# Kernel tuning notes

Hardware: AMD Instinct MI355X
Metric: run time of the kernel (lower is better)

Reference implementation:

```python
import jax, jax.numpy as jnp
import numpy as np

N_NODES = 100000
N_EDGES = 1250000
D_IN = 64
D_HID = 64
N_CLS = 40


def setup_inputs() -> dict:
    key = jax.random.key(0)
    ks = jax.random.split(key, 8)
    x = jax.random.normal(ks[0], (N_NODES, D_IN), dtype=jnp.float32)
    edge_index = jax.random.randint(ks[1], (2, N_EDGES), 0, N_NODES, dtype=jnp.int64)
    s = 1.0 / np.sqrt(D_IN)
    W1_l = jax.random.normal(ks[2], (D_IN, D_HID), dtype=jnp.float32) * s
    W1_r = jax.random.normal(ks[3], (D_IN, D_HID), dtype=jnp.float32) * s
    b1 = jnp.zeros((D_HID,), dtype=jnp.float32)
    s2 = 1.0 / np.sqrt(D_HID)
    W2_l = jax.random.normal(ks[4], (D_HID, N_CLS), dtype=jnp.float32) * s2
    W2_r = jax.random.normal(ks[5], (D_HID, N_CLS), dtype=jnp.float32) * s2
    b2 = jnp.zeros((N_CLS,), dtype=jnp.float32)
    return {"x": x, "edge_index": edge_index, "W1_l": W1_l, "b1": b1,
            "W1_r": W1_r, "W2_l": W2_l, "b2": b2, "W2_r": W2_r}


def _sage_conv(h, src, dst, n_nodes, W_l, b, W_r):
    # mean-aggregate neighbor features: out[i] = mean_{(j->i)} h[j]
    msg = h[src]                                             # [E, d] gather
    agg = jax.ops.segment_sum(msg, dst, num_segments=n_nodes)  # [N, d] scatter-add
    deg = jax.ops.segment_sum(jnp.ones_like(dst, dtype=h.dtype), dst,
                              num_segments=n_nodes)
    agg = agg / jnp.maximum(deg, 1.0)[:, None]
    # lin_l(aggregated, bias) + lin_r(root, no bias)
    return agg @ W_l + b + h @ W_r


def reference(x, edge_index, W1_l, b1, W1_r, W2_l, b2, W2_r):
    n = x.shape[0]
    src, dst = edge_index[0], edge_index[1]
    h = jax.nn.relu(_sage_conv(x, src, dst, n, W1_l, b1, W1_r))
    # dropout is identity in eval mode (training=False)
    h = _sage_conv(h, src, dst, n, W2_l, b2, W2_r)
    return jax.nn.log_softmax(h, axis=1)
```

## Files before the change

kernel.cpp:

```cpp
#include <hip/hip_runtime.h>
#include <hip/hip_bf16.h>
#include <math.h>

#define N_NODES 100000
#define N_EDGES 1250000
#define D_IN    64
#define D_HID   64
#define N_CLS   40

#define NBUCK      500
#define BUCK_NODES 200
#define BUCK_CAP   2944
#define NBLK_STAGE 512
#define NBLK_GEMM1 1024
#define ELL_W      44
#define GNODES     100

typedef unsigned int uint;
typedef __attribute__((ext_vector_type(8))) short bf16x8;
typedef __attribute__((ext_vector_type(4))) float f32x4;

static __device__ __forceinline__ uint pack_bf16x2(float a, float b) {
    unsigned short ua = __builtin_bit_cast(unsigned short, __float2bfloat16(a));
    unsigned short ub = __builtin_bit_cast(unsigned short, __float2bfloat16(b));
    return (uint)ua | ((uint)ub << 16);
}
static __device__ __forceinline__ short f2bf(float f) {
    return (short)__builtin_bit_cast(unsigned short, __float2bfloat16(f));
}

__global__ __launch_bounds__(256, 3) void stage_and_gemm1(
    const int* __restrict__ src, const int* __restrict__ dst,
    int* __restrict__ bucketCnt, uint* __restrict__ staged,
    const float* __restrict__ x,
    const float* __restrict__ W_l, const float* __restrict__ W_r,
    const float* __restrict__ b,
    __hip_bfloat16* __restrict__ y1, __hip_bfloat16* __restrict__ r1,
    int ntiles)
{
    __shared__ int cntB[NBUCK], offB[NBUCK], gbase[NBUCK];

    if (blockIdx.x < NBLK_STAGE) {
        const int per = (N_EDGES + NBLK_STAGE - 1) / NBLK_STAGE;
        const int e0 = blockIdx.x * per;
        const int e1 = (e0 + per < N_EDGES) ? e0 + per : N_EDGES;
        for (int i = threadIdx.x; i < NBUCK; i += 256) { cntB[i] = 0; offB[i] = 0; }
        __syncthreads();
        for (int e = e0 + threadIdx.x; e < e1; e += 256)
            atomicAdd(&cntB[dst[e] / BUCK_NODES], 1);
        __syncthreads();
        for (int i = threadIdx.x; i < NBUCK; i += 256) {
            int c = cntB[i];
            gbase[i] = c ? atomicAdd(&bucketCnt[i], c) : 0;
        }
        __syncthreads();
        for (int e = e0 + threadIdx.x; e < e1; e += 256) {
            int d = dst[e];
            int s = src[e];
            int bk = d / BUCK_NODES;
            int pos = gbase[bk] + atomicAdd(&offB[bk], 1);
            if (pos < BUCK_CAP)
                staged[(size_t)bk * BUCK_CAP + pos] =
                    (uint)s | ((uint)(d - bk * BUCK_NODES) << 17);
        }
        return;
    }

    const int gbid = blockIdx.x - NBLK_STAGE;
    if (gbid == 0 && threadIdx.x < 64)
        y1[(size_t)N_NODES * 64 + threadIdx.x] = __float2bfloat16(0.0f);

    const int lane = threadIdx.x & 63;
    const int m = lane & 15;
    const int q = lane >> 4;

    bf16x8 bfrag[8][2];
    float  biasv[4];
    #pragma unroll
    for (int t = 0; t < 8; ++t) {
        const float* Wsrc = (t < 4) ? W_l : W_r;
        const int c = t * 16 + m - ((t < 4) ? 0 : 64);
        #pragma unroll
        for (int ks = 0; ks < 2; ++ks) {
            bf16x8 f;
            #pragma unroll
            for (int j = 0; j < 8; ++j)
                f[j] = f2bf(Wsrc[(ks * 32 + q * 8 + j) * 64 + c]);
            bfrag[t][ks] = f;
        }
    }
    #pragma unroll
    for (int t = 0; t < 4; ++t) biasv[t] = b[t * 16 + m];

    int wid = gbid * 4 + (threadIdx.x >> 6);
    const int nw = NBLK_GEMM1 * 4;
    for (int tile = wid; tile < ntiles; tile += nw) {
        const int node0 = tile * 16;
        const float* xrow = x + (size_t)(node0 + m) * 64 + q * 8;
        bf16x8 afrag[2];
        #pragma unroll
        for (int ks = 0; ks < 2; ++ks) {
            float4 f0 = *(const float4*)(xrow + ks * 32);
            float4 f1 = *(const float4*)(xrow + ks * 32 + 4);
            bf16x8 a;
            a[0] = f2bf(f0.x); a[1] = f2bf(f0.y); a[2] = f2bf(f0.z); a[3] = f2bf(f0.w);
            a[4] = f2bf(f1.x); a[5] = f2bf(f1.y); a[6] = f2bf(f1.z); a[7] = f2bf(f1.w);
            afrag[ks] = a;
        }
        f32x4 acc[8];
        #pragma unroll
        for (int t = 0; t < 8; ++t) acc[t] = (f32x4){0.f, 0.f, 0.f, 0.f};
        #pragma unroll
        for (int ks = 0; ks < 2; ++ks) {
            #pragma unroll
            for (int t = 0; t < 8; ++t)
                acc[t] = __builtin_amdgcn_mfma_f32_16x16x32_bf16(
                    afrag[ks], bfrag[t][ks], acc[t], 0, 0, 0);
        }
        #pragma unroll
        for (int t = 0; t < 8; ++t) {
            #pragma unroll
            for (int r = 0; r < 4; ++r) {
                const size_t row = (size_t)(node0 + q * 4 + r);
                if (t < 4)
                    y1[row * 64 + t * 16 + m] = __float2bfloat16(acc[t][r]);
                else
                    r1[row * 64 + (t - 4) * 16 + m] =
                        __float2bfloat16(acc[t][r] + biasv[t - 4]);
            }
        }
    }
}

__global__ __launch_bounds__(512) void bucket_gather1(
    const __hip_bfloat16* __restrict__ y1,
    const uint* __restrict__ staged, const int* __restrict__ bucketCnt,
    __hip_bfloat16* __restrict__ h)
{
    __shared__ int lcnt[GNODES];
    __shared__ int lslots[GNODES * ELL_W + 64];
    const int pb = blockIdx.x >> 1;
    const int hf = blockIdx.x & 1;
    const int node0 = pb * BUCK_NODES + hf * GNODES;

    for (int i = threadIdx.x; i < GNODES; i += 512) lcnt[i] = 0;
    __syncthreads();

    int total = bucketCnt[pb]; if (total > BUCK_CAP) total = BUCK_CAP;
    const uint* sp = staged + (size_t)pb * BUCK_CAP;
    const int rel0 = hf * GNODES;
    for (int i = threadIdx.x; i < total; i += 512) {
        uint v = sp[i];
        int rel = (int)(v >> 17) - rel0;
        if (0 <= rel && rel < GNODES) {
            int pos = atomicAdd(&lcnt[rel], 1);
            if (pos < ELL_W) lslots[rel * ELL_W + pos] = (int)(v & 0x1FFFFu);
        }
    }
    __syncthreads();

    const int lane = threadIdx.x & 63;
    const int wv   = threadIdx.x >> 6;
    const int q4   = (lane >> 4) * 4;
    const int pre  = (lane & 15) * 8;
    const char* y1c = (const char*)y1;

    for (int n = wv; n < GNODES; n += 8) {
        const int node = node0 + n;
        const int degr = lcnt[n];
        const int idxv = lslots[n * ELL_W + lane];
        const int degc = degr < ELL_W ? degr : ELL_W;
        int idx = (lane >= degc) ? N_NODES : idxv;

        float a0 = 0.f, a1 = 0.f, a2 = 0.f, a3 = 0.f;
        const int groups = (degc + 15) & ~15;
        for (int e = 0; e < groups; e += 16) {
            int sel0 = __builtin_amdgcn_ds_bpermute(e * 4      + q4, idx);
            int sel1 = __builtin_amdgcn_ds_bpermute(e * 4 + 16 + q4, idx);
            int sel2 = __builtin_amdgcn_ds_bpermute(e * 4 + 32 + q4, idx);
            int sel3 = __builtin_amdgcn_ds_bpermute(e * 4 + 48 + q4, idx);
            uint2 d0 = *(const uint2*)(y1c + ((size_t)(uint)sel0 * 128u + (uint)pre));
            uint2 d1 = *(const uint2*)(y1c + ((size_t)(uint)sel1 * 128u + (uint)pre));
            uint2 d2 = *(const uint2*)(y1c + ((size_t)(uint)sel2 * 128u + (uint)pre));
            uint2 d3 = *(const uint2*)(y1c + ((size_t)(uint)sel3 * 128u + (uint)pre));
            a0 += __uint_as_float(d0.x << 16) + __uint_as_float(d1.x << 16)
                + __uint_as_float(d2.x << 16) + __uint_as_float(d3.x << 16);
            a1 += __uint_as_float(d0.x & 0xffff0000u) + __uint_as_float(d1.x & 0xffff0000u)
                + __uint_as_float(d2.x & 0xffff0000u) + __uint_as_float(d3.x & 0xffff0000u);
            a2 += __uint_as_float(d0.y << 16) + __uint_as_float(d1.y << 16)
                + __uint_as_float(d2.y << 16) + __uint_as_float(d3.y << 16);
            a3 += __uint_as_float(d0.y & 0xffff0000u) + __uint_as_float(d1.y & 0xffff0000u)
                + __uint_as_float(d2.y & 0xffff0000u) + __uint_as_float(d3.y & 0xffff0000u);
        }
        a0 += __shfl_xor(a0, 16); a0 += __shfl_xor(a0, 32);
        a1 += __shfl_xor(a1, 16); a1 += __shfl_xor(a1, 32);
        a2 += __shfl_xor(a2, 16); a2 += __shfl_xor(a2, 32);
        a3 += __shfl_xor(a3, 16); a3 += __shfl_xor(a3, 32);

        uint2 rr = *(const uint2*)((const char*)h + ((size_t)node * 128u + (uint)pre));
        float r0  = __uint_as_float(rr.x << 16);
        float r1v = __uint_as_float(rr.x & 0xffff0000u);
        float r2v = __uint_as_float(rr.y << 16);
        float r3  = __uint_as_float(rr.y & 0xffff0000u);

        float inv = 1.0f / (float)(degr > 1 ? degr : 1);
        float v0 = a0 * inv + r0;  v0 = v0 > 0.f ? v0 : 0.f;
        float v1 = a1 * inv + r1v; v1 = v1 > 0.f ? v1 : 0.f;
        float v2 = a2 * inv + r2v; v2 = v2 > 0.f ? v2 : 0.f;
        float v3 = a3 * inv + r3;  v3 = v3 > 0.f ? v3 : 0.f;

        if (lane < 16) {
            uint2 o;
            o.x = pack_bf16x2(v0, v1);
            o.y = pack_bf16x2(v2, v3);
            *(uint2*)((char*)h + ((size_t)node * 128u + (uint)pre)) = o;
        }
    }
}

__global__ __launch_bounds__(256, 3) void gemm2_mfma(
    const __hip_bfloat16* __restrict__ h,
    const float* __restrict__ W_l, const float* __restrict__ W_r,
    const float* __restrict__ b,
    __hip_bfloat16* __restrict__ y2, __hip_bfloat16* __restrict__ r2,
    int ntiles)
{
    if (blockIdx.x == 0 && threadIdx.x < N_CLS)
        y2[(size_t)N_NODES * N_CLS + threadIdx.x] = __float2bfloat16(0.0f);

    const int lane = threadIdx.x & 63;
    const int m = lane & 15;
    const int q = lane >> 4;

    bf16x8 bfrag[5][2];
    float  biasv[5];
    #pragma unroll
    for (int t = 0; t < 5; ++t) {
        const int g = t * 16 + m;
        const float* Wsrc = (g < N_CLS) ? W_l : W_r;
        const int c = (g < N_CLS) ? g : g - N_CLS;
        #pragma unroll
        for (int ks = 0; ks < 2; ++ks) {
            bf16x8 f;
            #pragma unroll
            for (int j = 0; j < 8; ++j)
                f[j] = f2bf(Wsrc[(ks * 32 + q * 8 + j) * N_CLS + c]);
            bfrag[t][ks] = f;
        }
        biasv[t] = (g >= N_CLS) ? b[g - N_CLS] : 0.0f;
    }

    int wid = blockIdx.x * 4 + (threadIdx.x >> 6);
    const int nw = gridDim.x * 4;
    for (int tile = wid; tile < ntiles; tile += nw) {
        const int node0 = tile * 16;
        const __hip_bfloat16* hrow = h + (size_t)(node0 + m) * 64 + q * 8;
        bf16x8 afrag[2];
        afrag[0] = *(const bf16x8*)(hrow);
        afrag[1] = *(const bf16x8*)(hrow + 32);
        f32x4 acc[5];
        #pragma unroll
        for (int t = 0; t < 5; ++t) acc[t] = (f32x4){0.f, 0.f, 0.f, 0.f};
        #pragma unroll
        for (int ks = 0; ks < 2; ++ks) {
            #pragma unroll
            for (int t = 0; t < 5; ++t)
                acc[t] = __builtin_amdgcn_mfma_f32_16x16x32_bf16(
                    afrag[ks], bfrag[t][ks], acc[t], 0, 0, 0);
        }
        #pragma unroll
        for (int t = 0; t < 5; ++t) {
            const int g = t * 16 + m;
            #pragma unroll
            for (int r = 0; r < 4; ++r) {
                const size_t row = (size_t)(node0 + q * 4 + r);
                float v = acc[t][r] + biasv[t];
                if (g < N_CLS) y2[row * N_CLS + g] = __float2bfloat16(v);
                else           r2[row * N_CLS + (g - N_CLS)] = __float2bfloat16(v);
            }
        }
    }
}

__global__ __launch_bounds__(512) void bucket_gather2(
    const __hip_bfloat16* __restrict__ y2,
    const __hip_bfloat16* __restrict__ r2,
    const uint* __restrict__ staged, const int* __restrict__ bucketCnt,
    float* __restrict__ out)
{
    __shared__ int lcnt[GNODES];
    __shared__ int lslots[GNODES * ELL_W + 64];
    const int pb = blockIdx.x >> 1;
    const int hf = blockIdx.x & 1;
    const int node0 = pb * BUCK_NODES + hf * GNODES;

    for (int i = threadIdx.x; i < GNODES; i += 512) lcnt[i] = 0;
    __syncthreads();

    int total = bucketCnt[pb]; if (total > BUCK_CAP) total = BUCK_CAP;
    const uint* sp = staged + (size_t)pb * BUCK_CAP;
    const int rel0 = hf * GNODES;
    for (int i = threadIdx.x; i < total; i += 512) {
        uint v = sp[i];
        int rel = (int)(v >> 17) - rel0;
        if (0 <= rel && rel < GNODES) {
            int pos = atomicAdd(&lcnt[rel], 1);
            if (pos < ELL_W) lslots[rel * ELL_W + pos] = (int)(v & 0x1FFFFu);
        }
    }
    __syncthreads();

    const int lane  = threadIdx.x & 63;
    const int wv    = threadIdx.x >> 6;
    const int lpair = lane & 31;
    const int p2    = (lane >> 5) * 4;
    const uint pre2 = (uint)(lpair < 20 ? lpair : 19) * 4u;
    const char* y2c = (const char*)y2;

    for (int n = wv; n < GNODES; n += 8) {
        const int node = node0 + n;
        const int degr = lcnt[n];
        const int idxv = lslots[n * ELL_W + lane];
        const int degc = degr < ELL_W ? degr : ELL_W;
        int idx = (lane >= degc) ? N_NODES : idxv;

        float a0 = 0.f, a1 = 0.f;
        const int groups = (degc + 7) & ~7;
        for (int e = 0; e < groups; e += 8) {
            int sel0 = __builtin_amdgcn_ds_bpermute(e * 4      + p2, idx);
            int sel1 = __builtin_amdgcn_ds_bpermute(e * 4 +  8 + p2, idx);
            int sel2 = __builtin_amdgcn_ds_bpermute(e * 4 + 16 + p2, idx);
            int sel3 = __builtin_amdgcn_ds_bpermute(e * 4 + 24 + p2, idx);
            uint d0 = *(const uint*)(y2c + ((size_t)(uint)sel0 * 80u + pre2));
            uint d1 = *(const uint*)(y2c + ((size_t)(uint)sel1 * 80u + pre2));
            uint d2 = *(const uint*)(y2c + ((size_t)(uint)sel2 * 80u + pre2));
            uint d3 = *(const uint*)(y2c + ((size_t)(uint)sel3 * 80u + pre2));
            a0 += __uint_as_float(d0 << 16) + __uint_as_float(d1 << 16)
                + __uint_as_float(d2 << 16) + __uint_as_float(d3 << 16);
            a1 += __uint_as_float(d0 & 0xffff0000u) + __uint_as_float(d1 & 0xffff0000u)
                + __uint_as_float(d2 & 0xffff0000u) + __uint_as_float(d3 & 0xffff0000u);
        }
        a0 += __shfl_xor(a0, 32);
        a1 += __shfl_xor(a1, 32);

        uint rr = *(const uint*)((const char*)r2 + ((size_t)node * 80u + pre2));
        float r0 = __uint_as_float(rr << 16);
        float r1 = __uint_as_float(rr & 0xffff0000u);

        float inv = 1.0f / (float)(degr > 1 ? degr : 1);
        float l0 = a0 * inv + r0;
        float l1 = a1 * inv + r1;
        if (lpair >= 20) { l0 = -INFINITY; l1 = -INFINITY; }

        float m = fmaxf(l0, l1);
        #pragma unroll
        for (int off = 16; off > 0; off >>= 1)
            m = fmaxf(m, __shfl_xor(m, off));
        float ex = (lpair < 20) ? (expf(l0 - m) + expf(l1 - m)) : 0.0f;
        #pragma unroll
        for (int off = 16; off > 0; off >>= 1)
            ex += __shfl_xor(ex, off);
        float lg = m + logf(ex);
        if (lane < 20) {
            float2 o = make_float2(l0 - lg, l1 - lg);
            *(float2*)(out + (size_t)node * N_CLS + lpair * 2) = o;
        }
    }
}

extern "C" void kernel_launch(void* const* d_in, const int* in_sizes, int n_in,
                              void* d_out, int out_size, void* d_ws, size_t ws_size,
                              hipStream_t stream)
{
    (void)in_sizes; (void)n_in; (void)out_size; (void)ws_size;

    const float* x    = (const float*)d_in[0];
    const int*   ei   = (const int*)d_in[1];
    const float* W1_l = (const float*)d_in[2];
    const float* b1   = (const float*)d_in[3];
    const float* W1_r = (const float*)d_in[4];
    const float* W2_l = (const float*)d_in[5];
    const float* b2   = (const float*)d_in[6];
    const float* W2_r = (const float*)d_in[7];
    float* out = (float*)d_out;

    const int* src = ei;
    const int* dst = ei + N_EDGES;

    char* ws = (char*)d_ws;
    int*            bucketCnt = (int*)(ws);
    uint*           staged    = (uint*)(ws + (1u << 20));
    __hip_bfloat16* y1        = (__hip_bfloat16*)(ws + 8388608u);
    __hip_bfloat16* y2        = (__hip_bfloat16*)(ws + 8388608u);
    __hip_bfloat16* h         = (__hip_bfloat16*)(ws + 22020096u);
    __hip_bfloat16* r2        = (__hip_bfloat16*)(ws + 35651584u);

    const int ntiles = N_NODES / 16;

    hipMemsetAsync(bucketCnt, 0, NBUCK * sizeof(int), stream);
    stage_and_gemm1<<<NBLK_STAGE + NBLK_GEMM1, 256, 0, stream>>>(
        src, dst, bucketCnt, staged, x, W1_l, W1_r, b1, y1, h, ntiles);

    bucket_gather1<<<NBUCK * 2, 512, 0, stream>>>(y1, staged, bucketCnt, h);

    gemm2_mfma<<<1024, 256, 0, stream>>>(h, W2_l, W2_r, b2, y2, r2, ntiles);

    bucket_gather2<<<NBUCK * 2, 512, 0, stream>>>(y2, r2, staged, bucketCnt, out);
}
```

Baseline: 194.0 us.

## Fuse layer-1 gather with layer-2 GEMM via LDS and add dynamic tile scheduling

Merges the layer-1 neighbor aggregation and the layer-2 MFMA GEMM into one kernel. Each block writes its 128 aggregated hidden rows into padded LDS and multiplies them there, so h no longer makes a round trip through global memory and one launch is dropped. Buckets grow to 256 nodes so bucket indexing becomes a shift. Staging blocks now also join the GEMM1 tile loop, which pulls tiles from an atomic counter. The cost is extra LDS per block, which may lower occupancy, and bounds checks for the partial last bucket.

```diff
diff --git a/kernel.cpp b/kernel.cpp
--- a/kernel.cpp
+++ b/kernel.cpp
@@ -8,13 +8,14 @@
 #define D_HID   64
 #define N_CLS   40
 
-#define NBUCK      500
-#define BUCK_NODES 200
-#define BUCK_CAP   2944
+#define NBUCK      391
+#define BUCK_NODES 256
+#define BUCK_CAP   3712
 #define NBLK_STAGE 512
 #define NBLK_GEMM1 1024
 #define ELL_W      44
-#define GNODES     100
+#define GNODES     128
+#define HPAD       80
 
 typedef unsigned int uint;
 typedef __attribute__((ext_vector_type(8))) short bf16x8;
@@ -31,12 +32,13 @@
 
 __global__ __launch_bounds__(256, 3) void stage_and_gemm1(
     const int* __restrict__ src, const int* __restrict__ dst,
-    int* __restrict__ bucketCnt, uint* __restrict__ staged,
+    int* __restrict__ bucketCnt, int* __restrict__ tileCtr,
+    uint* __restrict__ staged,
     const float* __restrict__ x,
     const float* __restrict__ W_l, const float* __restrict__ W_r,
     const float* __restrict__ b,
     __hip_bfloat16* __restrict__ y1, __hip_bfloat16* __restrict__ r1,
-    int ntiles)
+    __hip_bfloat16* __restrict__ y2, int ntiles)
 {
     __shared__ int cntB[NBUCK], offB[NBUCK], gbase[NBUCK];
 
@@ -47,7 +49,7 @@
         for (int i = threadIdx.x; i < NBUCK; i += 256) { cntB[i] = 0; offB[i] = 0; }
         __syncthreads();
         for (int e = e0 + threadIdx.x; e < e1; e += 256)
-            atomicAdd(&cntB[dst[e] / BUCK_NODES], 1);
+            atomicAdd(&cntB[dst[e] >> 8], 1);
         __syncthreads();
         for (int i = threadIdx.x; i < NBUCK; i += 256) {
             int c = cntB[i];
@@ -57,18 +59,17 @@
         for (int e = e0 + threadIdx.x; e < e1; e += 256) {
             int d = dst[e];
             int s = src[e];
-            int bk = d / BUCK_NODES;
+            int bk = d >> 8;
             int pos = gbase[bk] + atomicAdd(&offB[bk], 1);
             if (pos < BUCK_CAP)
                 staged[(size_t)bk * BUCK_CAP + pos] =
-                    (uint)s | ((uint)(d - bk * BUCK_NODES) << 17);
-        }
-        return;
-    }
-
-    const int gbid = blockIdx.x - NBLK_STAGE;
-    if (gbid == 0 && threadIdx.x < 64)
+                    (uint)s | ((uint)(d & 255) << 17);
+        }
+    } else if (blockIdx.x == NBLK_STAGE && threadIdx.x < 64) {
         y1[(size_t)N_NODES * 64 + threadIdx.x] = __float2bfloat16(0.0f);
+        if (threadIdx.x < N_CLS)
+            y2[(size_t)N_NODES * N_CLS + threadIdx.x] = __float2bfloat16(0.0f);
+    }
 
     const int lane = threadIdx.x & 63;
     const int m = lane & 15;
@@ -92,53 +93,63 @@
     #pragma unroll
     for (int t = 0; t < 4; ++t) biasv[t] = b[t * 16 + m];
 
-    int wid = gbid * 4 + (threadIdx.x >> 6);
-    const int nw = NBLK_GEMM1 * 4;
-    for (int tile = wid; tile < ntiles; tile += nw) {
-        const int node0 = tile * 16;
-        const float* xrow = x + (size_t)(node0 + m) * 64 + q * 8;
-        bf16x8 afrag[2];
-        #pragma unroll
-        for (int ks = 0; ks < 2; ++ks) {
-            float4 f0 = *(const float4*)(xrow + ks * 32);
-            float4 f1 = *(const float4*)(xrow + ks * 32 + 4);
-            bf16x8 a;
-            a[0] = f2bf(f0.x); a[1] = f2bf(f0.y); a[2] = f2bf(f0.z); a[3] = f2bf(f0.w);
-            a[4] = f2bf(f1.x); a[5] = f2bf(f1.y); a[6] = f2bf(f1.z); a[7] = f2bf(f1.w);
-            afrag[ks] = a;
-        }
-        f32x4 acc[8];
-        #pragma unroll
-        for (int t = 0; t < 8; ++t) acc[t] = (f32x4){0.f, 0.f, 0.f, 0.f};
-        #pragma unroll
-        for (int ks = 0; ks < 2; ++ks) {
-            #pragma unroll
-            for (int t = 0; t < 8; ++t)
-                acc[t] = __builtin_amdgcn_mfma_f32_16x16x32_bf16(
-                    afrag[ks], bfrag[t][ks], acc[t], 0, 0, 0);
-        }
-        #pragma unroll
-        for (int t = 0; t < 8; ++t) {
-            #pragma unroll
-            for (int r = 0; r < 4; ++r) {
-                const size_t row = (size_t)(node0 + q * 4 + r);
-                if (t < 4)
-                    y1[row * 64 + t * 16 + m] = __float2bfloat16(acc[t][r]);
-                else
-                    r1[row * 64 + (t - 4) * 16 + m] =
-                        __float2bfloat16(acc[t][r] + biasv[t - 4]);
+    for (;;) {
+        int t0 = 0;
+        if (lane == 0) t0 = atomicAdd(tileCtr, 8);
+        t0 = __shfl(t0, 0);
+        if (t0 >= ntiles) break;
+        const int tend = (t0 + 8 < ntiles) ? t0 + 8 : ntiles;
+        for (int tile = t0; tile < tend; ++tile) {
+            const int node0 = tile * 16;
+            const float* xrow = x + (size_t)(node0 + m) * 64 + q * 8;
+            bf16x8 afrag[2];
+            #pragma unroll
+            for (int ks = 0; ks < 2; ++ks) {
+                float4 f0 = *(const float4*)(xrow + ks * 32);
+                float4 f1 = *(const float4*)(xrow + ks * 32 + 4);
+                bf16x8 a;
+                a[0] = f2bf(f0.x); a[1] = f2bf(f0.y); a[2] = f2bf(f0.z); a[3] = f2bf(f0.w);
+                a[4] = f2bf(f1.x); a[5] = f2bf(f1.y); a[6] = f2bf(f1.z); a[7] = f2bf(f1.w);
+                afrag[ks] = a;
             }
-        }
-    }
-}
-
-__global__ __launch_bounds__(512) void bucket_gather1(
+            f32x4 acc[8];
+            #pragma unroll
+            for (int t = 0; t < 8; ++t) acc[t] = (f32x4){0.f, 0.f, 0.f, 0.f};
+            #pragma unroll
+            for (int ks = 0; ks < 2; ++ks) {
+                #pragma unroll
+                for (int t = 0; t < 8; ++t)
+                    acc[t] = __builtin_amdgcn_mfma_f32_16x16x32_bf16(
+                        afrag[ks], bfrag[t][ks], acc[t], 0, 0, 0);
+            }
+            #pragma unroll
+            for (int t = 0; t < 8; ++t) {
+                #pragma unroll
+                for (int r = 0; r < 4; ++r) {
+                    const size_t row = (size_t)(node0 + q * 4 + r);
+                    if (t < 4)
+                        y1[row * 64 + t * 16 + m] = __float2bfloat16(acc[t][r]);
+                    else
+                        r1[row * 64 + (t - 4) * 16 + m] =
+                            __float2bfloat16(acc[t][r] + biasv[t - 4]);
+                }
+            }
+        }
+    }
+}
+
+__global__ __launch_bounds__(512, 2) void gather1_gemm2(
     const __hip_bfloat16* __restrict__ y1,
     const uint* __restrict__ staged, const int* __restrict__ bucketCnt,
-    __hip_bfloat16* __restrict__ h)
+    const __hip_bfloat16* __restrict__ r1,
+    const float* __restrict__ W_l, const float* __restrict__ W_r,
+    const float* __restrict__ b,
+    __hip_bfloat16* __restrict__ y2, __hip_bfloat16* __restrict__ r2)
 {
-    __shared__ int lcnt[GNODES];
-    __shared__ int lslots[GNODES * ELL_W + 64];
+    __shared__ int   lcnt[GNODES];
+    __shared__ int   lslots[GNODES * ELL_W + 64];
+    __shared__ short hls[GNODES * HPAD];
+
     const int pb = blockIdx.x >> 1;
     const int hf = blockIdx.x & 1;
     const int node0 = pb * BUCK_NODES + hf * GNODES;
@@ -167,6 +178,7 @@
 
     for (int n = wv; n < GNODES; n += 8) {
         const int node = node0 + n;
+        if (node >= N_NODES) continue;
         const int degr = lcnt[n];
         const int idxv = lslots[n * ELL_W + lane];
         const int degc = degr < ELL_W ? degr : ELL_W;
@@ -197,7 +209,7 @@
         a2 += __shfl_xor(a2, 16); a2 += __shfl_xor(a2, 32);
         a3 += __shfl_xor(a3, 16); a3 += __shfl_xor(a3, 32);
 
-        uint2 rr = *(const uint2*)((const char*)h + ((size_t)node * 128u + (uint)pre));
+        uint2 rr = *(const uint2*)((const char*)r1 + ((size_t)node * 128u + (uint)pre));
         float r0  = __uint_as_float(rr.x << 16);
         float r1v = __uint_as_float(rr.x & 0xffff0000u);
         float r2v = __uint_as_float(rr.y << 16);
@@ -213,25 +225,13 @@
             uint2 o;
             o.x = pack_bf16x2(v0, v1);
             o.y = pack_bf16x2(v2, v3);
-            *(uint2*)((char*)h + ((size_t)node * 128u + (uint)pre)) = o;
-        }
-    }
-}
-
-__global__ __launch_bounds__(256, 3) void gemm2_mfma(
-    const __hip_bfloat16* __restrict__ h,
-    const float* __restrict__ W_l, const float* __restrict__ W_r,
-    const float* __restrict__ b,
-    __hip_bfloat16* __restrict__ y2, __hip_bfloat16* __restrict__ r2,
-    int ntiles)
-{
-    if (blockIdx.x == 0 && threadIdx.x < N_CLS)
-        y2[(size_t)N_NODES * N_CLS + threadIdx.x] = __float2bfloat16(0.0f);
-
-    const int lane = threadIdx.x & 63;
+            *(uint2*)(&hls[n * HPAD + (lane & 15) * 4]) = o;
+        }
+    }
+    __syncthreads();
+
     const int m = lane & 15;
     const int q = lane >> 4;
-
     bf16x8 bfrag[5][2];
     float  biasv[5];
     #pragma unroll
@@ -250,33 +250,31 @@
         biasv[t] = (g >= N_CLS) ? b[g - N_CLS] : 0.0f;
     }
 
-    int wid = blockIdx.x * 4 + (threadIdx.x >> 6);
-    const int nw = gridDim.x * 4;
-    for (int tile = wid; tile < ntiles; tile += nw) {
-        const int node0 = tile * 16;
-        const __hip_bfloat16* hrow = h + (size_t)(node0 + m) * 64 + q * 8;
-        bf16x8 afrag[2];
-        afrag[0] = *(const bf16x8*)(hrow);
-        afrag[1] = *(const bf16x8*)(hrow + 32);
-        f32x4 acc[5];
-        #pragma unroll
-        for (int t = 0; t < 5; ++t) acc[t] = (f32x4){0.f, 0.f, 0.f, 0.f};
-        #pragma unroll
-        for (int ks = 0; ks < 2; ++ks) {
-            #pragma unroll
-            for (int t = 0; t < 5; ++t)
-                acc[t] = __builtin_amdgcn_mfma_f32_16x16x32_bf16(
-                    afrag[ks], bfrag[t][ks], acc[t], 0, 0, 0);
-        }
-        #pragma unroll
-        for (int t = 0; t < 5; ++t) {
-            const int g = t * 16 + m;
-            #pragma unroll
-            for (int r = 0; r < 4; ++r) {
-                const size_t row = (size_t)(node0 + q * 4 + r);
+    const int trow0 = wv * 16;
+    bf16x8 afrag[2];
+    afrag[0] = *(const bf16x8*)(&hls[(trow0 + m) * HPAD + q * 8]);
+    afrag[1] = *(const bf16x8*)(&hls[(trow0 + m) * HPAD + 32 + q * 8]);
+    f32x4 acc[5];
+    #pragma unroll
+    for (int t = 0; t < 5; ++t) acc[t] = (f32x4){0.f, 0.f, 0.f, 0.f};
+    #pragma unroll
+    for (int ks = 0; ks < 2; ++ks) {
+        #pragma unroll
+        for (int t = 0; t < 5; ++t)
+            acc[t] = __builtin_amdgcn_mfma_f32_16x16x32_bf16(
+                afrag[ks], bfrag[t][ks], acc[t], 0, 0, 0);
+    }
+    const int gnode0 = node0 + trow0;
+    #pragma unroll
+    for (int t = 0; t < 5; ++t) {
+        const int g = t * 16 + m;
+        #pragma unroll
+        for (int r = 0; r < 4; ++r) {
+            const int row = gnode0 + q * 4 + r;
+            if (row < N_NODES) {
                 float v = acc[t][r] + biasv[t];
-                if (g < N_CLS) y2[row * N_CLS + g] = __float2bfloat16(v);
-                else           r2[row * N_CLS + (g - N_CLS)] = __float2bfloat16(v);
+                if (g < N_CLS) y2[(size_t)row * N_CLS + g] = __float2bfloat16(v);
+                else           r2[(size_t)row * N_CLS + (g - N_CLS)] = __float2bfloat16(v);
             }
         }
     }
@@ -319,6 +317,7 @@
 
     for (int n = wv; n < GNODES; n += 8) {
         const int node = node0 + n;
+        if (node >= N_NODES) continue;
         const int degr = lcnt[n];
         const int idxv = lslots[n * ELL_W + lane];
         const int degc = degr < ELL_W ? degr : ELL_W;
@@ -389,21 +388,22 @@
 
     char* ws = (char*)d_ws;
     int*            bucketCnt = (int*)(ws);
-    uint*           staged    = (uint*)(ws + (1u << 20));
+    int*            tileCtr   = (int*)(ws + 2048);
+    uint*           staged    = (uint*)(ws + 1048576u);
     __hip_bfloat16* y1        = (__hip_bfloat16*)(ws + 8388608u);
-    __hip_bfloat16* y2        = (__hip_bfloat16*)(ws + 8388608u);
-    __hip_bfloat16* h         = (__hip_bfloat16*)(ws + 22020096u);
-    __hip_bfloat16* r2        = (__hip_bfloat16*)(ws + 35651584u);
+    __hip_bfloat16* r1        = (__hip_bfloat16*)(ws + 22020096u);
+    __hip_bfloat16* y2        = (__hip_bfloat16*)(ws + 35651584u);
+    __hip_bfloat16* r2        = (__hip_bfloat16*)(ws + 45088768u);
 
     const int ntiles = N_NODES / 16;
 
-    hipMemsetAsync(bucketCnt, 0, NBUCK * sizeof(int), stream);
+    hipMemsetAsync(ws, 0, 4096, stream);
+
     stage_and_gemm1<<<NBLK_STAGE + NBLK_GEMM1, 256, 0, stream>>>(
-        src, dst, bucketCnt, staged, x, W1_l, W1_r, b1, y1, h, ntiles);
-
-    bucket_gather1<<<NBUCK * 2, 512, 0, stream>>>(y1, staged, bucketCnt, h);
-
-    gemm2_mfma<<<1024, 256, 0, stream>>>(h, W2_l, W2_r, b2, y2, r2, ntiles);
+        src, dst, bucketCnt, tileCtr, staged, x, W1_l, W1_r, b1, y1, r1, y2, ntiles);
+
+    gather1_gemm2<<<NBUCK * 2, 512, 0, stream>>>(
+        y1, staged, bucketCnt, r1, W2_l, W2_r, b2, y2, r2);
 
     bucket_gather2<<<NBUCK * 2, 512, 0, stream>>>(y2, r2, staged, bucketCnt, out);
 }
```

New measurement: 282.4 us. 1.46x slower.
